# Performance work log

Hardware: AMD Instinct MI355X
Metric: run time of the kernel (lower is better)

The kernel has to match this reference:

```python
import jax, jax.numpy as jnp
import numpy as np

D, H = 2048, 16
Q_RANK, KV_RANK = 1536, 512
NOPE, ROPE_D, V_D = 128, 64, 128
QK_D = NOPE + ROPE_D  # 192
S, B = 2048, 1
THETA = 10000.0
EPS = 1e-5


def rmsnorm(x, w, eps=EPS):
    return x * jax.lax.rsqrt(jnp.mean(x * x, -1, keepdims=True) + eps) * w


def rope_cos_sin(s, d, theta=THETA):
    inv = 1.0 / (theta ** (jnp.arange(0, d, 2, dtype=jnp.float32) / d))
    f = jnp.arange(s, dtype=jnp.float32)[:, None] * inv[None, :]  # [s, d//2]
    emb = jnp.concatenate([f, f], -1)  # [s, d]
    return jnp.cos(emb), jnp.sin(emb)


def apply_rope(x, cos, sin):
    # DeepSeek-V3 variant: de-interleave consecutive pairs into [even | odd] halves first
    b, h, s, d = x.shape
    x = x.reshape(b, h, s, d // 2, 2).transpose(0, 1, 2, 4, 3).reshape(b, h, s, d)
    x1, x2 = jnp.split(x, 2, -1)
    rot = jnp.concatenate([-x2, x1], -1)
    return x * cos + rot * sin


def setup_inputs() -> dict:
    key = jax.random.key(0)
    ks = jax.random.split(key, 10)
    s = 0.02
    return {
        "x": jax.random.normal(ks[0], (S, B, D), jnp.float32),
        "norm1_w": jnp.ones((D,), jnp.float32),
        "q_a_w": jax.random.normal(ks[1], (D, Q_RANK), jnp.float32) * s,
        "q_a_ln_w": jnp.ones((Q_RANK,), jnp.float32),
        "q_b_w": jax.random.normal(ks[2], (Q_RANK, H * QK_D), jnp.float32) * s,
        "kv_a_w": jax.random.normal(ks[3], (D, KV_RANK + ROPE_D), jnp.float32) * s,
        "kv_a_ln_w": jnp.ones((KV_RANK,), jnp.float32),
        "kv_b_w": jax.random.normal(ks[4], (KV_RANK, H * (NOPE + V_D)), jnp.float32) * s,
        "o_w": jax.random.normal(ks[5], (H * V_D, D), jnp.float32) * s,
        "norm2_w": jnp.ones((D,), jnp.float32),
        "ffn_w1": jax.random.normal(ks[6], (D, 4 * D), jnp.float32) * s,
        "ffn_b1": jnp.zeros((4 * D,), jnp.float32),
        "ffn_w2": jax.random.normal(ks[7], (4 * D, D), jnp.float32) * s,
        "ffn_b2": jnp.zeros((D,), jnp.float32),
    }


def reference(x, norm1_w, q_a_w, q_a_ln_w, q_b_w, kv_a_w, kv_a_ln_w, kv_b_w, o_w,
              norm2_w, ffn_w1, ffn_b1, ffn_w2, ffn_b2):
    # x: [S, B, D] (block transposes to [B, S, D] before MLA)
    hs = jnp.swapaxes(rmsnorm(x, norm1_w), 0, 1)  # [B, S, D]
    b, s, _ = hs.shape

    # --- MLA: low-rank Q and KV with decoupled RoPE ---
    q = rmsnorm(hs @ q_a_w, q_a_ln_w) @ q_b_w                    # [B, S, H*192]
    q = q.reshape(b, s, H, QK_D).transpose(0, 2, 1, 3)           # [B, H, S, 192]
    q_nope, q_pe = q[..., :NOPE], q[..., NOPE:]

    kv_a = hs @ kv_a_w                                           # [B, S, 576]
    c_kv, k_pe = kv_a[..., :KV_RANK], kv_a[..., KV_RANK:]        # [B,S,512], [B,S,64]
    kv = rmsnorm(c_kv, kv_a_ln_w) @ kv_b_w                       # [B, S, H*256]
    kv = kv.reshape(b, s, H, NOPE + V_D).transpose(0, 2, 1, 3)   # [B, H, S, 256]
    k_nope, v = kv[..., :NOPE], kv[..., NOPE:]

    cos, sin = rope_cos_sin(s, ROPE_D)
    q_pe = apply_rope(q_pe, cos, sin)                            # [B, H, S, 64]
    k_pe = apply_rope(k_pe[:, None, :, :], cos, sin)             # [B, 1, S, 64]

    q_full = jnp.concatenate([q_nope, q_pe], -1)                 # [B, H, S, 192]
    k_full = jnp.concatenate([k_nope, jnp.broadcast_to(k_pe, (b, H, s, ROPE_D))], -1)

    scores = jnp.einsum('bhqd,bhkd->bhqk', q_full, k_full) * (1.0 / np.sqrt(QK_D))
    causal = jnp.tril(jnp.ones((s, s), bool))
    scores = jnp.where(causal, scores, jnp.finfo(scores.dtype).min)
    attn = jax.nn.softmax(scores, -1)
    out = jnp.einsum('bhqk,bhkd->bhqd', attn, v)                 # [B, H, S, 128]
    out = out.transpose(0, 2, 1, 3).reshape(b, s, H * V_D) @ o_w # [B, S, D]

    x = x + jnp.swapaxes(out, 0, 1)                              # residual, back to [S,B,D]

    # --- FFN (exact GELU) ---
    h2 = rmsnorm(x, norm2_w)
    ffn = jax.nn.gelu(h2 @ ffn_w1 + ffn_b1, approximate=False) @ ffn_w2 + ffn_b2
    return x + ffn
```

## Files before the change

kernel.cpp:

```cpp
#include <hip/hip_runtime.h>
#include <hip/hip_bf16.h>

typedef __hip_bfloat16 bf16;
using bf16x8 = __attribute__((ext_vector_type(8))) __bf16;
using f32x4  = __attribute__((ext_vector_type(4))) float;

#define S_   2048
#define D_   2048
#define H_   16
#define QR_  1536
#define KVR_ 512
#define NOPE_ 128
#define ROPE_ 64
#define VD_  128
#define QKD_ 192
#define EPS_ 1e-5f
#define QKVN 2112

#define GLDS16(g, l) \
    __builtin_amdgcn_global_load_lds((const __attribute__((address_space(1))) void*)(g), \
                                     (__attribute__((address_space(3))) void*)(l), 16, 0, 0)

#define PIPE_WAIT4 asm volatile("s_waitcnt vmcnt(4)\n\ts_barrier" ::: "memory")
#define PIPE_WAIT0 asm volatile("s_waitcnt vmcnt(0)\n\ts_barrier" ::: "memory")

__global__ __launch_bounds__(256) void gemm_k(
    const bf16* __restrict__ A, const bf16* __restrict__ BT, void* __restrict__ Cv,
    const float* __restrict__ bias, const float* __restrict__ res,
    int M, int N, int K, int lda, int ldb, int ldc,
    long long strideA, long long strideB, long long strideC,
    int mode, int causal, int ksplit, int kchunk)
{
    int bn = blockIdx.x, bm = blockIdx.y;
    int bzC = blockIdx.z;
    int bz = bzC, kc = 0;
    if (ksplit > 1) { kc = bzC % ksplit; bz = bzC / ksplit; }
    if (causal == 1 && bn > bm) return;
    A  += (size_t)bz * strideA;
    BT += (size_t)bz * strideB;

    int k_end = K;
    if (causal == 2) { int kl = (bm + 1) * 128; if (kl < k_end) k_end = kl; }
    int k_begin = kc * kchunk;
    if (k_begin + kchunk < k_end) k_end = k_begin + kchunk;
    if (k_begin >= k_end) return;
    int nIter = (k_end - k_begin) >> 5;

    __shared__ bf16 sA[3 * 128 * 32];
    __shared__ bf16 sB[3 * 128 * 32];

    int tid  = threadIdx.x;
    int lane = tid & 63, wave = tid >> 6;
    int wr = wave >> 1, wc = wave & 1;
    int fr = lane & 15, fq = lane >> 4;

    int row0 = bm * 128, col0 = bn * 128;

    int srow = wave * 16 + (lane >> 2);
    int sko  = (lane & 3) * 8;
    const bf16* ga0 = A + (size_t)(row0 + srow) * lda + sko;
    const bf16* ga1 = ga0 + (size_t)64 * lda;
    int bn0 = col0 + srow;      if (bn0 > N - 1) bn0 = N - 1;
    int bn1 = col0 + srow + 64; if (bn1 > N - 1) bn1 = N - 1;
    const bf16* gb0 = BT + (size_t)bn0 * ldb + sko;
    const bf16* gb1 = BT + (size_t)bn1 * ldb + sko;
    bf16* lA0 = &sA[(wave * 16) * 32];
    bf16* lA1 = &sA[(64 + wave * 16) * 32];
    bf16* lB0 = &sB[(wave * 16) * 32];
    bf16* lB1 = &sB[(64 + wave * 16) * 32];

#define STAGE(ofs, k0) do {                  \
        GLDS16(ga0 + (k0), lA0 + (ofs));     \
        GLDS16(ga1 + (k0), lA1 + (ofs));     \
        GLDS16(gb0 + (k0), lB0 + (ofs));     \
        GLDS16(gb1 + (k0), lB1 + (ofs));     \
    } while (0)

    f32x4 acc[4][4] = {};

#define COMPUTE(ofs) do {                                                           \
        bf16x8 af[4], bv[4];                                                        \
        _Pragma("unroll")                                                           \
        for (int i = 0; i < 4; ++i)                                                 \
            af[i] = *(const bf16x8*)&sA[(ofs) + (wr*64 + i*16 + fr)*32 + fq*8];     \
        _Pragma("unroll")                                                           \
        for (int j = 0; j < 4; ++j)                                                 \
            bv[j] = *(const bf16x8*)&sB[(ofs) + (wc*64 + j*16 + fr)*32 + fq*8];     \
        _Pragma("unroll")                                                           \
        for (int i = 0; i < 4; ++i)                                                 \
            _Pragma("unroll")                                                       \
            for (int j = 0; j < 4; ++j)                                             \
                acc[i][j] = __builtin_amdgcn_mfma_f32_16x16x32_bf16(af[i], bv[j], acc[i][j], 0, 0, 0); \
    } while (0)

    STAGE(0, k_begin);
    if (nIter > 1) STAGE(4096, k_begin + 32);

    int curo = 0, pfo = 8192;
    int it = 0;
    for (; it < nIter - 1; ++it) {
        PIPE_WAIT4;
        if (it + 2 < nIter) STAGE(pfo, k_begin + (it + 2) * 32);
        COMPUTE(curo);
        curo += 4096; if (curo == 12288) curo = 0;
        pfo  += 4096; if (pfo  == 12288) pfo  = 0;
    }
    PIPE_WAIT0;
    COMPUTE(curo);
#undef STAGE
#undef COMPUTE

    #pragma unroll
    for (int i = 0; i < 4; ++i) {
        #pragma unroll
        for (int j = 0; j < 4; ++j) {
            int gc = col0 + wc*64 + j*16 + fr;
            if (gc >= N) continue;
            #pragma unroll
            for (int r = 0; r < 4; ++r) {
                int gr = row0 + wr*64 + i*16 + fq*4 + r;
                float v = acc[i][j][r];
                size_t off = (size_t)bzC * strideC + (size_t)gr * ldc + gc;
                if (mode == 0 || mode == 6) {
                    ((float*)Cv)[off] = v;
                } else if (mode == 1) {
                    ((bf16*)Cv)[off] = __float2bfloat16(v);
                } else if (mode == 2) {
                    ((float*)Cv)[off] = v + res[(size_t)gr * ldc + gc];
                } else if (mode == 3) {
                    float t = v + bias[gc];
                    t = 0.5f * t * (1.0f + erff(t * 0.70710678118654752f));
                    ((bf16*)Cv)[off] = __float2bfloat16(t);
                } else {
                    ((float*)Cv)[off] = v + bias[gc] + res[(size_t)gr * ldc + gc];
                }
            }
        }
    }
}

__global__ __launch_bounds__(512, 2) void gemm256_k(
    const bf16* __restrict__ A, const bf16* __restrict__ BT, void* __restrict__ Cv,
    const float* __restrict__ bias,
    int M, int N, int K, int lda, int ldb, int ldc,
    long long strideC, int mode, int kchunk)
{
    int bn = blockIdx.x, bm = blockIdx.y, kc = blockIdx.z;
    int k_begin = kc * kchunk;
    int k_end = (k_begin + kchunk < K) ? (k_begin + kchunk) : K;
    int NT = (k_end - k_begin) >> 6;

    __shared__ __align__(16) bf16 sA[2 * 256 * 64];
    __shared__ __align__(16) bf16 sB[2 * 256 * 64];

    int tid = threadIdx.x;
    int lane = tid & 63, w = tid >> 6;
    int wr = w >> 2, wc = w & 3;
    int fr = lane & 15, fq = lane >> 4;
    int row0 = bm * 256, col0 = bn * 256;

    int g0 = tid, g1 = tid + 512;
    int r0 = g0 >> 3, l0 = (g0 & 7) ^ (r0 & 7);
    int r1 = g1 >> 3, l1 = (g1 & 7) ^ (r1 & 7);
    const bf16* gA00 = A + (size_t)(row0 + r0) * lda + k_begin + l0 * 8;
    const bf16* gA01 = A + (size_t)(row0 + r1) * lda + k_begin + l1 * 8;
    const bf16* gA10 = gA00 + (size_t)128 * lda;
    const bf16* gA11 = gA01 + (size_t)128 * lda;
    int c00 = col0 + r0;       if (c00 > N - 1) c00 = N - 1;
    int c01 = col0 + r1;       if (c01 > N - 1) c01 = N - 1;
    int c10 = col0 + 128 + r0; if (c10 > N - 1) c10 = N - 1;
    int c11 = col0 + 128 + r1; if (c11 > N - 1) c11 = N - 1;
    const bf16* gB00 = BT + (size_t)c00 * ldb + k_begin + l0 * 8;
    const bf16* gB01 = BT + (size_t)c01 * ldb + k_begin + l1 * 8;
    const bf16* gB10 = BT + (size_t)c10 * ldb + k_begin + l0 * 8;
    const bf16* gB11 = BT + (size_t)c11 * ldb + k_begin + l1 * 8;

#define ST_HALF(arr, bofs, p0, p1, t) do {                                  \
        GLDS16((p0) + (size_t)(t) * 64, (arr) + (bofs) + w * 512);          \
        GLDS16((p1) + (size_t)(t) * 64, (arr) + (bofs) + w * 512 + 4096);   \
    } while (0)
#define ST_A0(b, t) ST_HALF(sA, (b) * 16384,        gA00, gA01, t)
#define ST_A1(b, t) ST_HALF(sA, (b) * 16384 + 8192, gA10, gA11, t)
#define ST_B0(b, t) ST_HALF(sB, (b) * 16384,        gB00, gB01, t)
#define ST_B1(b, t) ST_HALF(sB, (b) * 16384 + 8192, gB10, gB11, t)

    int arow = (wr * 128 + fr) * 64;
    int brow = (wc * 64 + fr) * 64;
    int pk0 = (fq ^ (fr & 7)) * 8;
    int pk1 = pk0 ^ 32;

    f32x4 acc[8][4] = {};

#define MFMA_QUAD(AF, IOFF, N0) do {                                        \
        __builtin_amdgcn_s_setprio(1);                                      \
        _Pragma("unroll")                                                   \
        for (int m = 0; m < 4; ++m) {                                       \
            _Pragma("unroll")                                               \
            for (int n = 0; n < 2; ++n) {                                   \
                acc[(IOFF)+m][(N0)+n] = __builtin_amdgcn_mfma_f32_16x16x32_bf16( \
                    AF[m][0], bfr[(N0)+n][0], acc[(IOFF)+m][(N0)+n], 0, 0, 0);   \
                acc[(IOFF)+m][(N0)+n] = __builtin_amdgcn_mfma_f32_16x16x32_bf16( \
                    AF[m][1], bfr[(N0)+n][1], acc[(IOFF)+m][(N0)+n], 0, 0, 0);   \
            }                                                               \
        }                                                                   \
        __builtin_amdgcn_s_setprio(0);                                      \
    } while (0)

    ST_A0(0, 0); ST_A1(0, 0); ST_B0(0, 0); ST_B1(0, 0);
    if (NT > 1) { ST_B0(1, 1); ST_B1(1, 1); ST_A0(1, 1); }
    if (NT > 1) asm volatile("s_waitcnt vmcnt(6)" ::: "memory");
    else        asm volatile("s_waitcnt vmcnt(0)" ::: "memory");
    __builtin_amdgcn_s_barrier();

    for (int t = 0; t < NT; ++t) {
        int buf = t & 1;
        int sbase = buf * 16384;
        bf16x8 aflo[4][2], afhi[4][2], bfr[4][2];

        #pragma unroll
        for (int m = 0; m < 4; ++m) {
            aflo[m][0] = *(const bf16x8*)&sA[sbase + arow + m*1024 + pk0];
            aflo[m][1] = *(const bf16x8*)&sA[sbase + arow + m*1024 + pk1];
        }
        #pragma unroll
        for (int n = 0; n < 4; ++n) {
            bfr[n][0] = *(const bf16x8*)&sB[sbase + brow + n*1024 + pk0];
            bfr[n][1] = *(const bf16x8*)&sB[sbase + brow + n*1024 + pk1];
        }
        if (t + 1 < NT) ST_A1((t + 1) & 1, t + 1);
        __builtin_amdgcn_s_barrier();
        asm volatile("s_waitcnt lgkmcnt(0)" ::: "memory");
        __builtin_amdgcn_sched_barrier(0);
        MFMA_QUAD(aflo, 0, 0);
        __builtin_amdgcn_s_barrier();

        #pragma unroll
        for (int m = 0; m < 4; ++m) {
            afhi[m][0] = *(const bf16x8*)&sA[sbase + arow + 4096 + m*1024 + pk0];
            afhi[m][1] = *(const bf16x8*)&sA[sbase + arow + 4096 + m*1024 + pk1];
        }
        if (t + 2 < NT) ST_B0(buf, t + 2);
        __builtin_amdgcn_s_barrier();
        MFMA_QUAD(aflo, 0, 2);
        __builtin_amdgcn_s_barrier();

        if (t + 2 < NT) ST_B1(buf, t + 2);
        __builtin_amdgcn_s_barrier();
        asm volatile("s_waitcnt lgkmcnt(0)" ::: "memory");
        __builtin_amdgcn_sched_barrier(0);
        MFMA_QUAD(afhi, 4, 0);
        __builtin_amdgcn_s_barrier();

        if (t + 2 < NT) ST_A0(buf, t + 2);
        if (t < NT - 2) asm volatile("s_waitcnt vmcnt(6)" ::: "memory");
        else            asm volatile("s_waitcnt vmcnt(0)" ::: "memory");
        __builtin_amdgcn_s_barrier();
        MFMA_QUAD(afhi, 4, 2);
        __builtin_amdgcn_s_barrier();
    }
#undef MFMA_QUAD
#undef ST_A0
#undef ST_A1
#undef ST_B0
#undef ST_B1
#undef ST_HALF

    #pragma unroll
    for (int i = 0; i < 8; ++i) {
        #pragma unroll
        for (int j = 0; j < 4; ++j) {
            int gc = col0 + wc*64 + j*16 + fr;
            if (gc >= N) continue;
            #pragma unroll
            for (int r = 0; r < 4; ++r) {
                int gr = row0 + wr*128 + i*16 + fq*4 + r;
                float v = acc[i][j][r];
                size_t off = (size_t)kc * strideC + (size_t)gr * ldc + gc;
                if (mode == 0 || mode == 6) {
                    ((float*)Cv)[off] = v;
                } else if (mode == 1) {
                    ((bf16*)Cv)[off] = __float2bfloat16(v);
                } else {
                    float tt = v + bias[gc];
                    tt = 0.5f * tt * (1.0f + erff(tt * 0.70710678118654752f));
                    ((bf16*)Cv)[off] = __float2bfloat16(tt);
                }
            }
        }
    }
}

__global__ __launch_bounds__(256) void red_k(const float* __restrict__ part,
        long long pstride4, int nch, const float* __restrict__ res,
        const float* __restrict__ bias, long long cols4,
        float* __restrict__ dstF, bf16* __restrict__ dstB, long long n4)
{
    long long i = (long long)blockIdx.x * 256 + threadIdx.x;
    long long stride = (long long)gridDim.x * 256;
    for (; i < n4; i += stride) {
        float4 v = ((const float4*)part)[i];
        for (int k = 1; k < nch; ++k) {
            float4 p = ((const float4*)part)[i + k * pstride4];
            v.x += p.x; v.y += p.y; v.z += p.z; v.w += p.w;
        }
        if (res) {
            float4 rr = ((const float4*)res)[i];
            v.x += rr.x; v.y += rr.y; v.z += rr.z; v.w += rr.w;
        }
        if (bias) {
            float4 b = ((const float4*)bias)[i % cols4];
            v.x += b.x; v.y += b.y; v.z += b.z; v.w += b.w;
        }
        if (dstB) {
            ushort4 o;
            bf16 t0 = __float2bfloat16(v.x); o.x = *(unsigned short*)&t0;
            bf16 t1 = __float2bfloat16(v.y); o.y = *(unsigned short*)&t1;
            bf16 t2 = __float2bfloat16(v.z); o.z = *(unsigned short*)&t2;
            bf16 t3 = __float2bfloat16(v.w); o.w = *(unsigned short*)&t3;
            ((ushort4*)dstB)[i] = o;
        } else {
            ((float4*)dstF)[i] = v;
        }
    }
}

__global__ __launch_bounds__(128) void pv_red(const float* __restrict__ part,
                                              bf16* __restrict__ ao, int grp)
{
    int r = blockIdx.x, head = blockIdx.y, d = threadIdx.x;
    int nv = ((r >> 7) + 4) >> 2;
    const float* p = part + ((size_t)head * 4) * S_ * VD_ + (size_t)r * VD_ + d;
    float s = 0.f;
    for (int k = 0; k < nv; ++k) s += p[(size_t)k * S_ * VD_];
    ao[(size_t)r * (H_ * VD_) + grp * 1024 + head * VD_ + d] = __float2bfloat16(s);
}

__global__ __launch_bounds__(256) void transpose_w(const float* __restrict__ in,
                                                   bf16* __restrict__ out, int R, int C)
{
    __shared__ float t[32][33];
    int c0 = blockIdx.x * 32, r0 = blockIdx.y * 32;
    int tx = threadIdx.x, ty = threadIdx.y;
    for (int j = ty; j < 32; j += 8) {
        int r = r0 + j, c = c0 + tx;
        t[j][tx] = (r < R && c < C) ? in[(size_t)r * C + c] : 0.f;
    }
    __syncthreads();
    for (int j = ty; j < 32; j += 8) {
        int c = c0 + j, r = r0 + tx;
        if (c < C && r < R) out[(size_t)c * R + r] = __float2bfloat16(t[tx][j]);
    }
}

__global__ __launch_bounds__(256) void transpose_v(const bf16* __restrict__ kv,
                                                   bf16* __restrict__ vT)
{
    __shared__ bf16 t[32][33];
    int h = blockIdx.z;
    int d0 = blockIdx.x * 32, s0 = blockIdx.y * 32;
    int tx = threadIdx.x, ty = threadIdx.y;
    for (int j = ty; j < 32; j += 8)
        t[j][tx] = kv[(size_t)(s0 + j) * (H_*256) + h*256 + 128 + d0 + tx];
    __syncthreads();
    for (int j = ty; j < 32; j += 8)
        vT[((size_t)h * VD_ + d0 + j) * S_ + s0 + tx] = t[tx][j];
}

__global__ __launch_bounds__(256) void rmsnorm_k(const float* __restrict__ in,
                                                 const float* __restrict__ w,
                                                 bf16* __restrict__ out,
                                                 int cols, int istride, int ostride)
{
    int row = blockIdx.x, tid = threadIdx.x;
    const float* ip = in + (size_t)row * istride;
    bf16* op = out + (size_t)row * ostride;
    float ss = 0.f;
    for (int c = tid; c < cols; c += 256) { float v = ip[c]; ss = fmaf(v, v, ss); }
    for (int o = 32; o > 0; o >>= 1) ss += __shfl_down(ss, o, 64);
    __shared__ float red[4];
    __shared__ float s_sc;
    int wave = tid >> 6, lane = tid & 63;
    if (lane == 0) red[wave] = ss;
    __syncthreads();
    if (tid == 0) s_sc = rsqrtf((red[0]+red[1]+red[2]+red[3]) / (float)cols + EPS_);
    __syncthreads();
    float sc = s_sc;
    for (int c = tid; c < cols; c += 256)
        op[c] = __float2bfloat16(ip[c] * sc * w[c]);
}

#define ROPE_LC 0.28782313662425575f

__global__ __launch_bounds__(192) void build_q(const bf16* __restrict__ q,
                                               bf16* __restrict__ qf)
{
    int s = blockIdx.x, h = blockIdx.y, t = threadIdx.x;
    const float scale = 0.07216878364870323f;
    const bf16* src = q + (size_t)s * (H_*QKD_) + h * QKD_;
    bf16* dst = qf + ((size_t)h * S_ + s) * QKD_;
    if (t < NOPE_) {
        dst[t] = __float2bfloat16(__bfloat162float(src[t]) * scale);
    } else {
        int i = (t - NOPE_) & 31;
        bool hi = (t - NOPE_) >= 32;
        float a = __bfloat162float(src[NOPE_ + 2*i]);
        float b = __bfloat162float(src[NOPE_ + 2*i + 1]);
        float inv = __expf(-(float)i * ROPE_LC);
        float f = (float)s * inv, c, sn;
        sincosf(f, &sn, &c);
        float v = hi ? (b * c + a * sn) : (a * c - b * sn);
        dst[t] = __float2bfloat16(v * scale);
    }
}

__global__ __launch_bounds__(192) void build_k(const bf16* __restrict__ kv,
                                               const float* __restrict__ qakva32,
                                               bf16* __restrict__ kf)
{
    int s = blockIdx.x, h = blockIdx.y, t = threadIdx.x;
    const bf16* src = kv + (size_t)s * (H_*256) + h * 256;
    bf16* dst = kf + ((size_t)h * S_ + s) * QKD_;
    if (t < NOPE_) {
        dst[t] = src[t];
    } else {
        int i = (t - NOPE_) & 31;
        bool hi = (t - NOPE_) >= 32;
        const float* pe = qakva32 + (size_t)s * QKVN + (QR_ + KVR_);
        float a = pe[2*i], b = pe[2*i + 1];
        float inv = __expf(-(float)i * ROPE_LC);
        float f = (float)s * inv, c, sn;
        sincosf(f, &sn, &c);
        dst[t] = __float2bfloat16(hi ? (b * c + a * sn) : (a * c - b * sn));
    }
}

__global__ __launch_bounds__(256) void softmax_k(bf16* __restrict__ Sc)
{
    int q = blockIdx.x, h = blockIdx.y;
    bf16* row = Sc + ((size_t)h * S_ + q) * S_;
    int n = q + 1;
    int klim = ((q >> 7) + 1) << 7;
    int tid = threadIdx.x, lane = tid & 63, wave = tid >> 6;
    __shared__ float red[4];
    __shared__ float bc;

    float v[8];
    #pragma unroll
    for (int k = 0; k < 8; ++k) {
        int c = tid + k * 256;
        v[k] = (c < n) ? __bfloat162float(row[c]) : -3.0e38f;
    }
    float mx = v[0];
    #pragma unroll
    for (int k = 1; k < 8; ++k) mx = fmaxf(mx, v[k]);
    for (int o = 32; o > 0; o >>= 1) mx = fmaxf(mx, __shfl_down(mx, o, 64));
    if (lane == 0) red[wave] = mx;
    __syncthreads();
    if (tid == 0) bc = fmaxf(fmaxf(red[0], red[1]), fmaxf(red[2], red[3]));
    __syncthreads();
    float m = bc;
    float sum = 0.f;
    #pragma unroll
    for (int k = 0; k < 8; ++k) {
        int c = tid + k * 256;
        v[k] = (c < n) ? __expf(v[k] - m) : 0.f;
        sum += v[k];
    }
    for (int o = 32; o > 0; o >>= 1) sum += __shfl_down(sum, o, 64);
    __syncthreads();
    if (lane == 0) red[wave] = sum;
    __syncthreads();
    if (tid == 0) bc = 1.0f / (red[0] + red[1] + red[2] + red[3]);
    __syncthreads();
    float inv = bc;
    #pragma unroll
    for (int k = 0; k < 8; ++k) {
        int c = tid + k * 256;
        if (c < klim) row[c] = __float2bfloat16(c < n ? v[k] * inv : 0.f);
    }
}

static inline void gemm(hipStream_t st, const bf16* A, const bf16* BT, void* C,
                        const float* bias, const float* res,
                        int M, int N, int K, int lda, int ldb, int ldc,
                        long long sA, long long sB, long long sC,
                        int batch, int mode, int causal, int ksplit = 1, int kchunk = 0)
{
    if (kchunk == 0) kchunk = K;
    dim3 g((N + 127) / 128, M / 128, batch * ksplit);
    gemm_k<<<g, 256, 0, st>>>(A, BT, C, bias, res, M, N, K, lda, ldb, ldc,
                              sA, sB, sC, mode, causal, ksplit, kchunk);
}

static inline void gemm256(hipStream_t st, const bf16* A, const bf16* BT, void* C,
                           const float* bias, int M, int N, int K,
                           int lda, int ldb, int ldc, long long sC,
                           int mode, int ksplit = 1, int kchunk = 0)
{
    if (kchunk == 0) kchunk = K;
    dim3 g((N + 255) / 256, M / 256, ksplit);
    gemm256_k<<<g, 512, 0, st>>>(A, BT, C, bias, M, N, K, lda, ldb, ldc,
                                 sC, mode, kchunk);
}

static inline void transw(hipStream_t st, const float* in, bf16* out, int R, int C)
{
    dim3 g((C + 31) / 32, (R + 31) / 32);
    transpose_w<<<g, dim3(32, 8), 0, st>>>(in, out, R, C);
}

extern "C" void kernel_launch(void* const* d_in, const int* in_sizes, int n_in,
                              void* d_out, int out_size, void* d_ws, size_t ws_size,
                              hipStream_t stream)
{
    const float* x        = (const float*)d_in[0];
    const float* norm1_w  = (const float*)d_in[1];
    const float* q_a_w    = (const float*)d_in[2];
    const float* q_a_ln_w = (const float*)d_in[3];
    const float* q_b_w    = (const float*)d_in[4];
    const float* kv_a_w   = (const float*)d_in[5];
    const float* kv_a_ln_w= (const float*)d_in[6];
    const float* kv_b_w   = (const float*)d_in[7];
    const float* o_w      = (const float*)d_in[8];
    const float* norm2_w  = (const float*)d_in[9];
    const float* ffn_w1   = (const float*)d_in[10];
    const float* ffn_b1   = (const float*)d_in[11];
    const float* ffn_w2   = (const float*)d_in[12];
    const float* ffn_b2   = (const float*)d_in[13];
    float* out = (float*)d_out;

    size_t off = 0;
    auto alloc = [&](size_t bytes) -> void* {
        void* p = (char*)d_ws + off;
        off += (bytes + 255) & ~(size_t)255;
        return p;
    };
    bf16*  hs     = (bf16*) alloc((size_t)S_*D_*2);
    bf16*  wqakvT = (bf16*) alloc((size_t)QKVN*D_*2);
    bf16*  wqbT   = (bf16*) alloc((size_t)(H_*QKD_)*QR_*2);
    bf16*  wkvbT  = (bf16*) alloc((size_t)(H_*(NOPE_+VD_))*KVR_*2);
    bf16*  woT    = (bf16*) alloc((size_t)D_*(H_*VD_)*2);
    bf16*  wf1T   = (bf16*) alloc((size_t)(4*D_)*D_*2);
    bf16*  wf2T   = (bf16*) alloc((size_t)D_*(4*D_)*2);
    float* qakva32= (float*)alloc((size_t)S_*QKVN*4);
    bf16*  qln    = (bf16*) alloc((size_t)S_*QR_*2);
    bf16*  kvln   = (bf16*) alloc((size_t)S_*KVR_*2);
    bf16*  qb     = (bf16*) alloc((size_t)S_*H_*QKD_*2);
    bf16*  kvb    = (bf16*) alloc((size_t)S_*H_*(NOPE_+VD_)*2);
    bf16*  qf     = (bf16*) alloc((size_t)H_*S_*QKD_*2);
    bf16*  kf     = (bf16*) alloc((size_t)H_*S_*QKD_*2);
    bf16*  vT     = (bf16*) alloc((size_t)H_*VD_*S_*2);
    bf16*  Sc     = (bf16*) alloc((size_t)8*S_*S_*2);
    float* qakvaP = (float*)Sc;
    float* qbP    = (float*)Sc;
    float* pvP    = (float*)qakva32;
    float* oP     = (float*)Sc;
    float* f2P    = (float*)d_ws;
    float* x2     = qakva32;
    bf16*  h2     = qb;
    bf16*  ao     = kvb;
    bf16*  a1     = Sc;

    transw(stream, q_a_w,  wqakvT,                    D_,  QR_);
    transw(stream, kv_a_w, wqakvT + (size_t)QR_ * D_, D_,  KVR_+ROPE_);
    transw(stream, q_b_w,  wqbT,  QR_, H_*QKD_);
    transw(stream, kv_b_w, wkvbT, KVR_, H_*(NOPE_+VD_));
    transw(stream, o_w,    woT,   H_*VD_, D_);
    transw(stream, ffn_w1, wf1T,  D_,  4*D_);
    transw(stream, ffn_w2, wf2T,  4*D_, D_);

    rmsnorm_k<<<S_, 256, 0, stream>>>(x, norm1_w, hs, D_, D_, D_);

    gemm256(stream, hs, wqakvT, qakvaP, nullptr, S_, QKVN, D_, D_, D_, QKVN,
            (long long)S_*QKVN, 6, 3, 768);
    red_k<<<1024, 256, 0, stream>>>(qakvaP, (long long)S_*QKVN/4, 3, nullptr, nullptr, 1,
                                    qakva32, nullptr, (long long)S_*QKVN/4);

    rmsnorm_k<<<S_, 256, 0, stream>>>(qakva32, q_a_ln_w, qln, QR_, QKVN, QR_);
    gemm256(stream, qln, wqbT, qbP, nullptr, S_, H_*QKD_, QR_, QR_, QR_, H_*QKD_,
            (long long)S_*(H_*QKD_), 6, 2, 768);
    red_k<<<1024, 256, 0, stream>>>(qbP, (long long)S_*(H_*QKD_)/4, 2, nullptr, nullptr, 1,
                                    nullptr, qb, (long long)S_*(H_*QKD_)/4);

    rmsnorm_k<<<S_, 256, 0, stream>>>(qakva32 + QR_, kv_a_ln_w, kvln, KVR_, QKVN, KVR_);
    gemm(stream, kvln, wkvbT, kvb, nullptr, nullptr, S_, H_*(NOPE_+VD_), KVR_,
         KVR_, KVR_, H_*(NOPE_+VD_), 0, 0, 0, 1, 1, 0);

    build_q<<<dim3(S_, H_), 192, 0, stream>>>(qb, qf);
    build_k<<<dim3(S_, H_), 192, 0, stream>>>(kvb, qakva32, kf);
    transpose_v<<<dim3(VD_/32, S_/32, H_), dim3(32, 8), 0, stream>>>(kvb, vT);

    for (int g = 0; g < 2; ++g) {
        const bf16* qfg = qf + (size_t)g * 8 * S_ * QKD_;
        const bf16* kfg = kf + (size_t)g * 8 * S_ * QKD_;
        const bf16* vTg = vT + (size_t)g * 8 * VD_ * S_;
        gemm(stream, qfg, kfg, Sc, nullptr, nullptr,
             S_, S_, QKD_, QKD_, QKD_, S_,
             (long long)S_*QKD_, (long long)S_*QKD_, (long long)S_*S_, 8, 1, 1);
        softmax_k<<<dim3(S_, 8), 256, 0, stream>>>(Sc);
        gemm(stream, Sc, vTg, pvP, nullptr, nullptr,
             S_, VD_, S_, S_, S_, VD_,
             (long long)S_*S_, (long long)VD_*S_, (long long)S_*VD_, 8, 6, 2, 4, 512);
        pv_red<<<dim3(S_, 8), 128, 0, stream>>>(pvP, ao, g);
    }

    gemm256(stream, ao, woT, oP, nullptr, S_, D_, H_*VD_, H_*VD_, H_*VD_, D_,
            (long long)S_*D_, 6, 4, 512);
    red_k<<<1024, 256, 0, stream>>>(oP, (long long)S_*D_/4, 4, x, nullptr, 1,
                                    x2, nullptr, (long long)S_*D_/4);

    rmsnorm_k<<<S_, 256, 0, stream>>>(x2, norm2_w, h2, D_, D_, D_);
    gemm256(stream, h2, wf1T, a1, ffn_b1, S_, 4*D_, D_, D_, D_, 4*D_,
            0, 3, 1, 0);
    gemm256(stream, a1, wf2T, f2P, nullptr, S_, D_, 4*D_, 4*D_, 4*D_, D_,
            (long long)S_*D_, 6, 4, 2048);
    red_k<<<1024, 256, 0, stream>>>(f2P, (long long)S_*D_/4, 4, x2, ffn_b2, D_/4,
                                    out, nullptr, (long long)S_*D_/4);
}
```

Before: 946.7 us.

## Fuse split-K reductions with RMSNorm/RoPE and vectorize weight transpose

Replaces the split-K reduce plus separate rmsnorm and build_q kernels with fused per-row kernels (reduce+dual RMSNorm+pe extract, reduce+RoPE/scale into qf, reduce+residual+RMSNorm). It also widens the weight transpose to float4 loads over 128-column tiles and adds extra lgkmcnt waits in the GEMM main loop. The aim is fewer launches and fewer round trips through global memory for intermediates. The added waits could serialize LDS traffic in the GEMM, and the fused kernels use one block per row with fewer blocks.

```diff
diff --git a/kernel.cpp b/kernel.cpp
--- a/kernel.cpp
+++ b/kernel.cpp
@@ -228,6 +228,7 @@
             bfr[n][1] = *(const bf16x8*)&sB[sbase + brow + n*1024 + pk1];
         }
         if (t + 1 < NT) ST_A1((t + 1) & 1, t + 1);
+        asm volatile("s_waitcnt lgkmcnt(8)" ::: "memory");
         __builtin_amdgcn_s_barrier();
         asm volatile("s_waitcnt lgkmcnt(0)" ::: "memory");
         __builtin_amdgcn_sched_barrier(0);
@@ -241,6 +242,8 @@
         }
         if (t + 2 < NT) ST_B0(buf, t + 2);
         __builtin_amdgcn_s_barrier();
+        asm volatile("s_waitcnt lgkmcnt(0)" ::: "memory");
+        __builtin_amdgcn_sched_barrier(0);
         MFMA_QUAD(aflo, 0, 2);
         __builtin_amdgcn_s_barrier();
 
@@ -324,6 +327,117 @@
     }
 }
 
+__global__ __launch_bounds__(256) void red_qakva_k(const float* __restrict__ part,
+        const float* __restrict__ qw, const float* __restrict__ kvw,
+        bf16* __restrict__ qln, bf16* __restrict__ kvln, float* __restrict__ pe)
+{
+    int row = blockIdx.x, tid = threadIdx.x;
+    const float* p0 = part + (size_t)row * QKVN;
+    const float* p1 = p0 + (size_t)S_ * QKVN;
+    const float* p2 = p1 + (size_t)S_ * QKVN;
+    float v[9];
+    float ssq_q = 0.f, ssq_kv = 0.f;
+    #pragma unroll
+    for (int k = 0; k < 9; ++k) {
+        int c = tid + k * 256;
+        float s = 0.f;
+        if (c < QKVN) s = p0[c] + p1[c] + p2[c];
+        v[k] = s;
+        if (c < QR_) ssq_q = fmaf(s, s, ssq_q);
+        else if (c < QR_ + KVR_) ssq_kv = fmaf(s, s, ssq_kv);
+    }
+    for (int o = 32; o > 0; o >>= 1) {
+        ssq_q  += __shfl_down(ssq_q,  o, 64);
+        ssq_kv += __shfl_down(ssq_kv, o, 64);
+    }
+    __shared__ float rq[4], rkv[4];
+    __shared__ float sq, skv;
+    int wave = tid >> 6, lane = tid & 63;
+    if (lane == 0) { rq[wave] = ssq_q; rkv[wave] = ssq_kv; }
+    __syncthreads();
+    if (tid == 0) {
+        sq  = rsqrtf((rq[0]+rq[1]+rq[2]+rq[3])   / (float)QR_  + EPS_);
+        skv = rsqrtf((rkv[0]+rkv[1]+rkv[2]+rkv[3]) / (float)KVR_ + EPS_);
+    }
+    __syncthreads();
+    float a = sq, b = skv;
+    #pragma unroll
+    for (int k = 0; k < 9; ++k) {
+        int c = tid + k * 256;
+        if (c < QR_) {
+            qln[(size_t)row * QR_ + c] = __float2bfloat16(v[k] * a * qw[c]);
+        } else if (c < QR_ + KVR_) {
+            kvln[(size_t)row * KVR_ + (c - QR_)] = __float2bfloat16(v[k] * b * kvw[c - QR_]);
+        } else if (c < QKVN) {
+            pe[(size_t)row * ROPE_ + (c - QR_ - KVR_)] = v[k];
+        }
+    }
+}
+
+#define ROPE_LC 0.28782313662425575f
+
+__global__ __launch_bounds__(256) void red_buildq_k(const float* __restrict__ part,
+                                                    bf16* __restrict__ qf)
+{
+    int s = blockIdx.x, tid = threadIdx.x;
+    const float* p0 = part + (size_t)s * (H_*QKD_);
+    const float* p1 = p0 + (size_t)S_ * (H_*QKD_);
+    __shared__ float rowv[H_*QKD_];
+    for (int c = tid; c < H_*QKD_; c += 256) rowv[c] = p0[c] + p1[c];
+    __syncthreads();
+    const float scale = 0.07216878364870323f;
+    for (int o = tid; o < H_*QKD_; o += 256) {
+        int h = o / QKD_, t = o - h*QKD_;
+        const float* src = rowv + h*QKD_;
+        float outv;
+        if (t < NOPE_) {
+            outv = src[t] * scale;
+        } else {
+            int i = (t - NOPE_) & 31;
+            bool hi = (t - NOPE_) >= 32;
+            float a = src[NOPE_ + 2*i], b = src[NOPE_ + 2*i + 1];
+            float inv = __expf(-(float)i * ROPE_LC);
+            float f = (float)s * inv, c2, sn;
+            sincosf(f, &sn, &c2);
+            outv = (hi ? (b * c2 + a * sn) : (a * c2 - b * sn)) * scale;
+        }
+        qf[((size_t)h * S_ + s) * QKD_ + t] = __float2bfloat16(outv);
+    }
+}
+
+__global__ __launch_bounds__(256) void red_o_rms_k(const float* __restrict__ part,
+        const float* __restrict__ x, const float* __restrict__ w,
+        float* __restrict__ x2, bf16* __restrict__ h2)
+{
+    int row = blockIdx.x, tid = threadIdx.x;
+    const float* p = part + (size_t)row * D_;
+    const long long pl = (long long)S_ * D_;
+    float v[8];
+    float ssq = 0.f;
+    #pragma unroll
+    for (int k = 0; k < 8; ++k) {
+        int c = tid + k * 256;
+        float s = p[c] + p[c + pl] + p[c + 2*pl] + p[c + 3*pl] + x[(size_t)row * D_ + c];
+        v[k] = s;
+        ssq = fmaf(s, s, ssq);
+        x2[(size_t)row * D_ + c] = s;
+    }
+    for (int o = 32; o > 0; o >>= 1) ssq += __shfl_down(ssq, o, 64);
+    __shared__ float red[4];
+    __shared__ float s_sc;
+    int wave = tid >> 6, lane = tid & 63;
+    if (lane == 0) red[wave] = ssq;
+    __syncthreads();
+    if (tid == 0) s_sc = rsqrtf((red[0]+red[1]+red[2]+red[3]) / (float)D_ + EPS_);
+    __syncthreads();
+    float sc = s_sc;
+    #pragma unroll
+    for (int k = 0; k < 8; ++k) {
+        int c = tid + k * 256;
+        h2[(size_t)row * D_ + c] = __float2bfloat16(v[k] * sc * w[c]);
+    }
+}
+
 __global__ __launch_bounds__(128) void pv_red(const float* __restrict__ part,
                                               bf16* __restrict__ ao, int grp)
 {
@@ -335,20 +449,34 @@
     ao[(size_t)r * (H_ * VD_) + grp * 1024 + head * VD_ + d] = __float2bfloat16(s);
 }
 
-__global__ __launch_bounds__(256) void transpose_w(const float* __restrict__ in,
-                                                   bf16* __restrict__ out, int R, int C)
-{
-    __shared__ float t[32][33];
-    int c0 = blockIdx.x * 32, r0 = blockIdx.y * 32;
+__global__ __launch_bounds__(256) void transpose_w4(const float* __restrict__ in,
+                                                    bf16* __restrict__ out, int R, int C)
+{
+    __shared__ float t[128][33];
+    int c0 = blockIdx.x * 128, r0 = blockIdx.y * 32;
     int tx = threadIdx.x, ty = threadIdx.y;
-    for (int j = ty; j < 32; j += 8) {
-        int r = r0 + j, c = c0 + tx;
-        t[j][tx] = (r < R && c < C) ? in[(size_t)r * C + c] : 0.f;
-    }
-    __syncthreads();
-    for (int j = ty; j < 32; j += 8) {
-        int c = c0 + j, r = r0 + tx;
-        if (c < C && r < R) out[(size_t)c * R + r] = __float2bfloat16(t[tx][j]);
+    #pragma unroll
+    for (int j = 0; j < 4; ++j) {
+        int r = r0 + ty + j*8;
+        int c = c0 + tx*4;
+        if (c + 3 < C) {
+            float4 v4 = *(const float4*)&in[(size_t)r * C + c];
+            t[tx*4+0][ty+j*8] = v4.x; t[tx*4+1][ty+j*8] = v4.y;
+            t[tx*4+2][ty+j*8] = v4.z; t[tx*4+3][ty+j*8] = v4.w;
+        } else {
+            #pragma unroll
+            for (int kk = 0; kk < 4; ++kk) {
+                int cc = c + kk;
+                t[tx*4+kk][ty+j*8] = (cc < C) ? in[(size_t)r * C + cc] : 0.f;
+            }
+        }
+    }
+    __syncthreads();
+    #pragma unroll
+    for (int j = 0; j < 16; ++j) {
+        int cl = ty + j*8;
+        int c = c0 + cl;
+        if (c < C) out[(size_t)c * R + r0 + tx] = __float2bfloat16(t[cl][tx]);
     }
 }
 
@@ -389,32 +517,8 @@
         op[c] = __float2bfloat16(ip[c] * sc * w[c]);
 }
 
-#define ROPE_LC 0.28782313662425575f
-
-__global__ __launch_bounds__(192) void build_q(const bf16* __restrict__ q,
-                                               bf16* __restrict__ qf)
-{
-    int s = blockIdx.x, h = blockIdx.y, t = threadIdx.x;
-    const float scale = 0.07216878364870323f;
-    const bf16* src = q + (size_t)s * (H_*QKD_) + h * QKD_;
-    bf16* dst = qf + ((size_t)h * S_ + s) * QKD_;
-    if (t < NOPE_) {
-        dst[t] = __float2bfloat16(__bfloat162float(src[t]) * scale);
-    } else {
-        int i = (t - NOPE_) & 31;
-        bool hi = (t - NOPE_) >= 32;
-        float a = __bfloat162float(src[NOPE_ + 2*i]);
-        float b = __bfloat162float(src[NOPE_ + 2*i + 1]);
-        float inv = __expf(-(float)i * ROPE_LC);
-        float f = (float)s * inv, c, sn;
-        sincosf(f, &sn, &c);
-        float v = hi ? (b * c + a * sn) : (a * c - b * sn);
-        dst[t] = __float2bfloat16(v * scale);
-    }
-}
-
 __global__ __launch_bounds__(192) void build_k(const bf16* __restrict__ kv,
-                                               const float* __restrict__ qakva32,
+                                               const float* __restrict__ pe,
                                                bf16* __restrict__ kf)
 {
     int s = blockIdx.x, h = blockIdx.y, t = threadIdx.x;
@@ -425,8 +529,8 @@
     } else {
         int i = (t - NOPE_) & 31;
         bool hi = (t - NOPE_) >= 32;
-        const float* pe = qakva32 + (size_t)s * QKVN + (QR_ + KVR_);
-        float a = pe[2*i], b = pe[2*i + 1];
+        const float* p = pe + (size_t)s * ROPE_;
+        float a = p[2*i], b = p[2*i + 1];
         float inv = __expf(-(float)i * ROPE_LC);
         float f = (float)s * inv, c, sn;
         sincosf(f, &sn, &c);
@@ -505,8 +609,8 @@
 
 static inline void transw(hipStream_t st, const float* in, bf16* out, int R, int C)
 {
-    dim3 g((C + 31) / 32, (R + 31) / 32);
-    transpose_w<<<g, dim3(32, 8), 0, st>>>(in, out, R, C);
+    dim3 g((C + 127) / 128, R / 32);
+    transpose_w4<<<g, dim3(32, 8), 0, st>>>(in, out, R, C);
 }
 
 extern "C" void kernel_launch(void* const* d_in, const int* in_sizes, int n_in,
@@ -550,6 +654,7 @@
     bf16*  qf     = (bf16*) alloc((size_t)H_*S_*QKD_*2);
     bf16*  kf     = (bf16*) alloc((size_t)H_*S_*QKD_*2);
     bf16*  vT     = (bf16*) alloc((size_t)H_*VD_*S_*2);
+    float* pe     = (float*)alloc((size_t)S_*ROPE_*4);
     bf16*  Sc     = (bf16*) alloc((size_t)8*S_*S_*2);
     float* qakvaP = (float*)Sc;
     float* qbP    = (float*)Sc;
@@ -573,21 +678,16 @@
 
     gemm256(stream, hs, wqakvT, qakvaP, nullptr, S_, QKVN, D_, D_, D_, QKVN,
             (long long)S_*QKVN, 6, 3, 768);
-    red_k<<<1024, 256, 0, stream>>>(qakvaP, (long long)S_*QKVN/4, 3, nullptr, nullptr, 1,
-                                    qakva32, nullptr, (long long)S_*QKVN/4);
-
-    rmsnorm_k<<<S_, 256, 0, stream>>>(qakva32, q_a_ln_w, qln, QR_, QKVN, QR_);
+    red_qakva_k<<<S_, 256, 0, stream>>>(qakvaP, q_a_ln_w, kv_a_ln_w, qln, kvln, pe);
+
     gemm256(stream, qln, wqbT, qbP, nullptr, S_, H_*QKD_, QR_, QR_, QR_, H_*QKD_,
             (long long)S_*(H_*QKD_), 6, 2, 768);
-    red_k<<<1024, 256, 0, stream>>>(qbP, (long long)S_*(H_*QKD_)/4, 2, nullptr, nullptr, 1,
-                                    nullptr, qb, (long long)S_*(H_*QKD_)/4);
-
-    rmsnorm_k<<<S_, 256, 0, stream>>>(qakva32 + QR_, kv_a_ln_w, kvln, KVR_, QKVN, KVR_);
+    red_buildq_k<<<S_, 256, 0, stream>>>(qbP, qf);
+
     gemm(stream, kvln, wkvbT, kvb, nullptr, nullptr, S_, H_*(NOPE_+VD_), KVR_,
          KVR_, KVR_, H_*(NOPE_+VD_), 0, 0, 0, 1, 1, 0);
 
-    build_q<<<dim3(S_, H_), 192, 0, stream>>>(qb, qf);
-    build_k<<<dim3(S_, H_), 192, 0, stream>>>(kvb, qakva32, kf);
+    build_k<<<dim3(S_, H_), 192, 0, stream>>>(kvb, pe, kf);
     transpose_v<<<dim3(VD_/32, S_/32, H_), dim3(32, 8), 0, stream>>>(kvb, vT);
 
     for (int g = 0; g < 2; ++g) {
@@ -606,10 +706,8 @@
 
     gemm256(stream, ao, woT, oP, nullptr, S_, D_, H_*VD_, H_*VD_, H_*VD_, D_,
             (long long)S_*D_, 6, 4, 512);
-    red_k<<<1024, 256, 0, stream>>>(oP, (long long)S_*D_/4, 4, x, nullptr, 1,
-                                    x2, nullptr, (long long)S_*D_/4);
-
-    rmsnorm_k<<<S_, 256, 0, stream>>>(x2, norm2_w, h2, D_, D_, D_);
+    red_o_rms_k<<<S_, 256, 0, stream>>>(oP, x, norm2_w, x2, h2);
+
     gemm256(stream, h2, wf1T, a1, ffn_b1, S_, 4*D_, D_, D_, D_, 4*D_,
             0, 3, 1, 0);
     gemm256(stream, a1, wf2T, f2P, nullptr, S_, D_, 4*D_, 4*D_, 4*D_, D_,
```

Result: faster. 905.0 us (-4.4%).
